# Kernel tuning notes

Hardware: AMD Instinct MI355X
Metric: run time of the kernel (lower is better)

Reference implementation:

```python
import jax, jax.numpy as jnp
import numpy as np

MAXLEN, BATCH, LATENT = 128, 32, 64
DT = 0.1
NSTEPS = 10  # steps = tf.range(0, 1, delta=DT)
HID = 32


def setup_inputs() -> dict:
    key = jax.random.key(0)
    k1, k2, k3 = jax.random.split(key, 3)
    embeddings = jax.random.normal(k1, (BATCH, MAXLEN, LATENT), dtype=jnp.float32)
    # score model: flatten(xt) ++ time -> Dense(32, relu) -> Dense(latent)
    W1 = jax.random.normal(k2, (MAXLEN * LATENT + 1, HID), dtype=jnp.float32) * 0.01
    b1 = jnp.zeros((HID,), jnp.float32)
    W2 = jax.random.normal(k3, (HID, LATENT), dtype=jnp.float32) * 0.001
    b2 = jnp.zeros((LATENT,), jnp.float32)
    return {"embeddings": embeddings, "W1": W1, "b1": b1, "W2": W2, "b2": b2}


def _score_fn(xt, t, W1, b1, W2, b2):
    # xt: (B', L, D), t: (B', 1) -> score (B', D)
    h = jnp.concatenate([xt.reshape(xt.shape[0], -1), t], axis=-1)
    h = jax.nn.relu(h @ W1 + b1)
    return h @ W2 + b2


def _forward(embeddings, W1, b1, W2, b2):
    L, B, D = MAXLEN, BATCH, LATENT
    idx = jnp.arange(L)
    emb_tr = jnp.transpose(embeddings, (1, 0, 2))                    # (L, B, D)
    # vectorized_masking (include=True): mask[t, j] = j < t
    mask = (idx[None, :] < idx[:, None]).astype(embeddings.dtype)    # (L_t, L_j)
    masked = mask[:, :, None, None] * emb_tr[None]                   # (L, L, B, D)
    score_input = masked.reshape(L, L * B, D).transpose(1, 0, 2)     # (L*B, L, D)
    labels = masked[idx, idx]                                        # (L, B, D) diagonal (zeros by construction)
    flat_pos = jnp.arange(B)[None, :] * L + idx[:, None]             # (L, B): index b*L + i

    def step(carry, xs):
        xt, error = carry
        t_val, key = xs
        t = jnp.full((L * B, 1), 1.0, embeddings.dtype) * t_val
        score = _score_fn(xt, t, W1, b1, W2, b2)                     # (L*B, D)
        snorm = jnp.linalg.norm(score)
        dW = jax.random.normal(key, (L * B, D), dtype=embeddings.dtype) * jnp.sqrt(jnp.asarray(DT, embeddings.dtype))
        dx = 0.5 * score * DT + snorm * dW
        xt_tr = xt.transpose(1, 0, 2)                                # (L, L*B, D)
        # update_slice_by_gather for every step i: xt_tr[i, b*L+i] += dx[b*L+i]
        xt_upd = xt_tr.at[idx[:, None], flat_pos].add(dx[flat_pos])  # (L, L*B, D)
        preds = xt_upd.reshape(L, L, B, D)[idx, idx]                 # gather_diagonal_slices -> (L, B, D)
        error = error + jnp.mean((labels - preds) ** 2, axis=-1)     # (L, B)
        return (xt_upd.transpose(1, 0, 2), error), None

    times = jnp.arange(NSTEPS, dtype=embeddings.dtype) * DT
    keys = jax.random.split(jax.random.key(42), NSTEPS)
    init = (score_input, jnp.zeros((L, B), embeddings.dtype))
    (xt_fin, error), _ = jax.lax.scan(step, init, (times, keys))
    xt = xt_fin.reshape(L, L, B, D)[idx, idx].transpose(1, 0, 2)     # (B, L, D)
    step_loss = jnp.sum(error)
    sequence_loss = jnp.mean(jnp.abs(embeddings - xt))
    return xt, step_loss, sequence_loss


def reference(embeddings, W1, b1, W2, b2):
    return _forward(embeddings, W1, b1, W2, b2)
```

## Files before the change

### kernel.cpp

```cpp
#include <hip/hip_runtime.h>
#include <stdint.h>

#define THREEFRY_PARTITIONABLE 1

#define DEV_HOST __host__ __device__

namespace {
constexpr int kNS      = 10;
constexpr int kSamples = 4096;
constexpr int kElems   = 262144;

constexpr int OFF_SUF   = 0;
constexpr int OFF_BASE  = 262144;
constexpr int OFF_U     = 393216;
constexpr int OFF_SCORE = 655360;
constexpr int OFF_SNRM  = 917504;
constexpr int OFF_LOSS  = 917514;
constexpr int WS_FLOATS = 917516;
}

DEV_HOST inline void tf2x32(uint32_t k0, uint32_t k1, uint32_t x0, uint32_t x1,
                            uint32_t& o0, uint32_t& o1) {
  const uint32_t k2 = k0 ^ k1 ^ 0x1BD11BDAu;
#define TF_R(r) { x0 += x1; x1 = (x1 << (r)) | (x1 >> (32 - (r))); x1 ^= x0; }
  x0 += k0; x1 += k1;
  TF_R(13) TF_R(15) TF_R(26) TF_R(6)
  x0 += k1; x1 += k2 + 1u;
  TF_R(17) TF_R(29) TF_R(16) TF_R(24)
  x0 += k2; x1 += k0 + 2u;
  TF_R(13) TF_R(15) TF_R(26) TF_R(6)
  x0 += k0; x1 += k1 + 3u;
  TF_R(17) TF_R(29) TF_R(16) TF_R(24)
  x0 += k1; x1 += k2 + 4u;
  TF_R(13) TF_R(15) TF_R(26) TF_R(6)
  x0 += k2; x1 += k0 + 5u;
#undef TF_R
  o0 = x0; o1 = x1;
}

__device__ inline uint32_t rand_bits(uint32_t key0, uint32_t key1, uint32_t idx) {
#if THREEFRY_PARTITIONABLE
  uint32_t y0, y1;
  tf2x32(key0, key1, 0u, idx, y0, y1);
  return y0 ^ y1;
#else
  const uint32_t half = kElems / 2;
  uint32_t y0, y1;
  if (idx < half) { tf2x32(key0, key1, idx, half + idx, y0, y1); return y0; }
  tf2x32(key0, key1, idx - half, idx, y0, y1);
  return y1;
#endif
}

__device__ inline float erfinv_xla(float x) {
  float w = -log1pf(-x * x);
  float p;
  if (w < 5.0f) {
    w = w - 2.5f;
    p = 2.81022636e-08f;
    p = fmaf(p, w, 3.43273939e-07f);
    p = fmaf(p, w, -3.5233877e-06f);
    p = fmaf(p, w, -4.39150654e-06f);
    p = fmaf(p, w, 0.00021858087f);
    p = fmaf(p, w, -0.00125372503f);
    p = fmaf(p, w, -0.00417768164f);
    p = fmaf(p, w, 0.246640727f);
    p = fmaf(p, w, 1.50140941f);
  } else {
    w = sqrtf(w) - 3.0f;
    p = -0.000200214257f;
    p = fmaf(p, w, 0.000100950558f);
    p = fmaf(p, w, 0.00134934322f);
    p = fmaf(p, w, -0.00367342844f);
    p = fmaf(p, w, 0.00573950773f);
    p = fmaf(p, w, -0.0076224613f);
    p = fmaf(p, w, 0.00943887047f);
    p = fmaf(p, w, 1.00167406f);
    p = fmaf(p, w, 2.83297682f);
  }
  return p * x;
}

__device__ inline float bits_to_normal(uint32_t bits) {
  const float lo = -0.99999994039535522f;
  float f = __uint_as_float((bits >> 9) | 0x3f800000u) - 1.0f;
  float u = fmaxf(lo, f * 2.0f + lo);
  return 1.41421356237309515f * erfinv_xla(u);
}

__global__ __launch_bounds__(256) void k_suffix(const float* __restrict__ W1,
                                                float* __restrict__ S) {
  const int p = blockIdx.x * 256 + threadIdx.x;
  if (p >= 2048) return;
  const int d = p >> 5, h = p & 31;
  float acc = 0.0f;
  S[(127 * 64 + d) * 32 + h] = 0.0f;
  for (int j = 126; j >= 0; --j) {
    acc += W1[((j + 1) * 64 + d) * 32 + h];
    S[(j * 64 + d) * 32 + h] = acc;
  }
}

__global__ __launch_bounds__(256) void k_base(const float* __restrict__ emb,
                                              const float* __restrict__ S,
                                              const float* __restrict__ b1,
                                              float* __restrict__ base) {
  const int tid = blockIdx.x * 256 + threadIdx.x;
  const int s = tid >> 5, h = tid & 31;
  const int j = s >> 5, b = s & 31;
  const float* e = emb + (b * 128 + j) * 64;
  float acc = b1[h];
  for (int d = 0; d < 64; ++d)
    acc = fmaf(e[d], S[(j * 64 + d) * 32 + h], acc);
  base[s * 32 + h] = acc;
}

__global__ __launch_bounds__(256) void k_step(
    const float* __restrict__ base, float* __restrict__ u,
    const float* __restrict__ W1, const float* __restrict__ W2,
    const float* __restrict__ b2, float* __restrict__ score,
    float* __restrict__ snorm_acc, float* __restrict__ loss_acc,
    int k, float tval, uint32_t key0, uint32_t key1) {
  __shared__ float u_sh[8][64];
  __shared__ float h_sh[8][32];
  __shared__ float wsum[4];
  const int tid = threadIdx.x;
  const int s0 = blockIdx.x * 8;

  if (k > 0) {
    const float snorm = sqrtf(snorm_acc[k - 1]);
#pragma unroll
    for (int r = 0; r < 2; ++r) {
      const int off = r * 256 + tid;
      const int e = s0 * 64 + off;
      const int s = s0 + (off >> 6);
      const float n = bits_to_normal(rand_bits(key0, key1, (uint32_t)e));
      const float dW = n * 0.31622776601683794f;
      const float dx = score[e] * 0.05f + snorm * dW;
      const float un = u[e] + dx;
      u[e] = un;
      u_sh[off >> 6][off & 63] = un;
      if ((s & 127) == (s >> 5)) {
        float sq = un * un;
#pragma unroll
        for (int o = 32; o > 0; o >>= 1) sq += __shfl_down(sq, o);
        if ((tid & 63) == 0) atomicAdd(&loss_acc[0], sq * (1.0f / 64.0f));
      }
    }
  } else {
#pragma unroll
    for (int r = 0; r < 2; ++r) {
      const int off = r * 256 + tid;
      u_sh[off >> 6][off & 63] = u[s0 * 64 + off];
    }
  }
  __syncthreads();

  {
    const int sl = tid >> 5, h = tid & 31;
    const int s = s0 + sl;
    const float* w1r = W1 + ((s & 127) * 64) * 32 + h;
    float pre = base[s * 32 + h] + tval * W1[8192 * 32 + h];
#pragma unroll 16
    for (int d = 0; d < 64; ++d)
      pre = fmaf(u_sh[sl][d], w1r[d * 32], pre);
    h_sh[sl][h] = fmaxf(pre, 0.0f);
  }
  __syncthreads();

  {
    const int sl = tid >> 5, c = tid & 31;
    const int s = s0 + sl;
    float sc0 = b2[c], sc1 = b2[c + 32];
#pragma unroll
    for (int hh = 0; hh < 32; ++hh) {
      const float hv = h_sh[sl][hh];
      sc0 = fmaf(hv, W2[hh * 64 + c], sc0);
      sc1 = fmaf(hv, W2[hh * 64 + c + 32], sc1);
    }
    score[s * 64 + c] = sc0;
    score[s * 64 + c + 32] = sc1;
    float sq = fmaf(sc0, sc0, sc1 * sc1);
#pragma unroll
    for (int o = 32; o > 0; o >>= 1) sq += __shfl_down(sq, o);
    if ((tid & 63) == 0) wsum[tid >> 6] = sq;
  }
  __syncthreads();
  if (tid == 0) atomicAdd(snorm_acc + k, wsum[0] + wsum[1] + wsum[2] + wsum[3]);
}

__global__ __launch_bounds__(256) void k_last(
    float* __restrict__ u, const float* __restrict__ score,
    const float* __restrict__ snorm_acc, float* __restrict__ loss_acc,
    uint32_t key0, uint32_t key1) {
  const int e = blockIdx.x * 256 + threadIdx.x;
  const int s = e >> 6;
  const float snorm = sqrtf(snorm_acc[kNS - 1]);
  const float n = bits_to_normal(rand_bits(key0, key1, (uint32_t)e));
  const float dx = score[e] * 0.05f + snorm * (n * 0.31622776601683794f);
  const float un = u[e] + dx;
  u[e] = un;
  if ((s & 127) == (s >> 5)) {
    float sq = un * un;
#pragma unroll
    for (int o = 32; o > 0; o >>= 1) sq += __shfl_down(sq, o);
    if ((threadIdx.x & 63) == 0) atomicAdd(&loss_acc[0], sq * (1.0f / 64.0f));
  }
}

__global__ __launch_bounds__(256) void k_final(const float* __restrict__ emb,
                                               const float* __restrict__ u,
                                               float* __restrict__ out,
                                               float* __restrict__ loss_acc) {
  const int g = blockIdx.x * 256 + threadIdx.x;
  const int d = g & 63, bi = g >> 6, i = bi & 127, b = bi >> 7;
  const int m = i * 32 + b;
  const int bp = m >> 7, t = m & 127;
  const int s = i * 32 + bp;
  float v = 0.0f;
  if (i < t) v = emb[(bp * 128 + i) * 64 + d];
  if ((s & 127) == t) v += u[s * 64 + d];
  out[g] = v;
  float ad = fabsf(emb[g] - v);
#pragma unroll
  for (int o = 32; o > 0; o >>= 1) ad += __shfl_down(ad, o);
  __shared__ float wsum[4];
  if ((threadIdx.x & 63) == 0) wsum[threadIdx.x >> 6] = ad;
  __syncthreads();
  if (threadIdx.x == 0) atomicAdd(&loss_acc[1], wsum[0] + wsum[1] + wsum[2] + wsum[3]);
}

__global__ void k_write(float* __restrict__ out, const float* __restrict__ loss_acc) {
  if (threadIdx.x == 0 && blockIdx.x == 0) {
    out[262144] = loss_acc[0];
    out[262145] = loss_acc[1] * (1.0f / 262144.0f);
  }
}

static void compute_step_keys(uint32_t keys[kNS][2]) {
#if THREEFRY_PARTITIONABLE
  for (int i = 0; i < kNS; ++i) {
    uint32_t y0, y1;
    tf2x32(0u, 42u, 0u, (uint32_t)i, y0, y1);
    keys[i][0] = y0; keys[i][1] = y1;
  }
#else
  uint32_t a[kNS], b[kNS], outw[2 * kNS];
  for (int i = 0; i < kNS; ++i)
    tf2x32(0u, 42u, (uint32_t)i, (uint32_t)(kNS + i), a[i], b[i]);
  for (int i = 0; i < kNS; ++i) { outw[i] = a[i]; outw[kNS + i] = b[i]; }
  for (int i = 0; i < kNS; ++i) { keys[i][0] = outw[2 * i]; keys[i][1] = outw[2 * i + 1]; }
#endif
}

extern "C" void kernel_launch(void* const* d_in, const int* in_sizes, int n_in,
                              void* d_out, int out_size, void* d_ws, size_t ws_size,
                              hipStream_t stream) {
  (void)in_sizes; (void)n_in; (void)out_size; (void)ws_size;
  const float* emb = (const float*)d_in[0];
  const float* W1  = (const float*)d_in[1];
  const float* b1  = (const float*)d_in[2];
  const float* W2  = (const float*)d_in[3];
  const float* b2  = (const float*)d_in[4];
  float* out = (float*)d_out;
  float* ws  = (float*)d_ws;

  float* S     = ws + OFF_SUF;
  float* base  = ws + OFF_BASE;
  float* u     = ws + OFF_U;
  float* score = ws + OFF_SCORE;
  float* snrm  = ws + OFF_SNRM;
  float* loss  = ws + OFF_LOSS;

  uint32_t keys[kNS][2];
  compute_step_keys(keys);

  hipMemsetAsync(u, 0, (size_t)(WS_FLOATS - OFF_U) * sizeof(float), stream);

  k_suffix<<<8, 256, 0, stream>>>(W1, S);
  k_base<<<512, 256, 0, stream>>>(emb, S, b1, base);

  for (int k = 0; k < kNS; ++k) {
    const float tval = (float)k * 0.1f;
    const uint32_t pk0 = (k > 0) ? keys[k - 1][0] : 0u;
    const uint32_t pk1 = (k > 0) ? keys[k - 1][1] : 0u;
    k_step<<<512, 256, 0, stream>>>(base, u, W1, W2, b2, score, snrm, loss,
                                    k, tval, pk0, pk1);
  }
  k_last<<<1024, 256, 0, stream>>>(u, score, snrm, loss, keys[kNS - 1][0], keys[kNS - 1][1]);
  k_final<<<1024, 256, 0, stream>>>(emb, u, out, loss);
  k_write<<<1, 64, 0, stream>>>(out, loss);
}
```

Baseline: 216.9 us.

## Fuse all SDE steps into one persistent kernel with software grid barriers

Replaces the per-step launches, the base/last/final/write kernels and the memset with one persistent 512-block kernel. Each block keeps its W1 slice, base projection and state u in registers across the ten steps. Software grid barriers built on atomic counters synchronise the global score norm between steps. The final gather and loss reduction also run inside the kernel, which removes launch overhead and the global round-trips of score and u. It relies on all 512 blocks being co-resident (launch_bounds 256,2 on a many-CU GPU); if they are not, the barrier deadlocks, and the 64-float register array per thread raises register pressure.

```diff
diff --git a/kernel.cpp b/kernel.cpp
--- a/kernel.cpp
+++ b/kernel.cpp
@@ -6,17 +6,17 @@
 #define DEV_HOST __host__ __device__
 
 namespace {
-constexpr int kNS      = 10;
-constexpr int kSamples = 4096;
-constexpr int kElems   = 262144;
-
-constexpr int OFF_SUF   = 0;
-constexpr int OFF_BASE  = 262144;
-constexpr int OFF_U     = 393216;
-constexpr int OFF_SCORE = 655360;
-constexpr int OFF_SNRM  = 917504;
-constexpr int OFF_LOSS  = 917514;
-constexpr int WS_FLOATS = 917516;
+constexpr int kNS = 10;
+constexpr int kNB = 512;
+
+constexpr int OFF_SUF     = 0;
+constexpr int OFF_U       = 262144;
+constexpr int OFF_SNRM    = 524288;
+constexpr int OFF_BAR     = 524300;
+constexpr int BAR_UINTS   = 12 * 8 * 16;
+constexpr int OFF_LOSSBLK = OFF_BAR + BAR_UINTS;
+constexpr int ZACC_N      = 12 + BAR_UINTS;
+constexpr int WS_FLOATS   = OFF_LOSSBLK + 2 * kNB;
 }
 
 DEV_HOST inline void tf2x32(uint32_t k0, uint32_t k1, uint32_t x0, uint32_t x1,
@@ -44,7 +44,7 @@
   tf2x32(key0, key1, 0u, idx, y0, y1);
   return y0 ^ y1;
 #else
-  const uint32_t half = kElems / 2;
+  const uint32_t half = 262144u / 2;
   uint32_t y0, y1;
   if (idx < half) { tf2x32(key0, key1, idx, half + idx, y0, y1); return y0; }
   tf2x32(key0, key1, idx - half, idx, y0, y1);
@@ -88,9 +88,33 @@
   return 1.41421356237309515f * erfinv_xla(u);
 }
 
+__device__ inline void gridbar(unsigned* b8, unsigned nblk, bool wait) {
+  __syncthreads();
+  if (threadIdx.x == 0) {
+    __threadfence();
+    __hip_atomic_fetch_add(b8 + (blockIdx.x & 7) * 16, 1u,
+                           __ATOMIC_RELEASE, __HIP_MEMORY_SCOPE_AGENT);
+    if (wait) {
+      for (;;) {
+        unsigned tot = 0;
+#pragma unroll
+        for (int i = 0; i < 8; ++i)
+          tot += __hip_atomic_load(b8 + i * 16, __ATOMIC_RELAXED,
+                                   __HIP_MEMORY_SCOPE_AGENT);
+        if (tot >= nblk) break;
+        __builtin_amdgcn_s_sleep(1);
+      }
+      __threadfence();
+    }
+  }
+  __syncthreads();
+}
+
 __global__ __launch_bounds__(256) void k_suffix(const float* __restrict__ W1,
-                                                float* __restrict__ S) {
+                                                float* __restrict__ S,
+                                                float* __restrict__ zacc) {
   const int p = blockIdx.x * 256 + threadIdx.x;
+  if (p < ZACC_N) zacc[p] = 0.0f;
   if (p >= 2048) return;
   const int d = p >> 5, h = p & 31;
   float acc = 0.0f;
@@ -101,139 +125,142 @@
   }
 }
 
-__global__ __launch_bounds__(256) void k_base(const float* __restrict__ emb,
-                                              const float* __restrict__ S,
-                                              const float* __restrict__ b1,
-                                              float* __restrict__ base) {
-  const int tid = blockIdx.x * 256 + threadIdx.x;
-  const int s = tid >> 5, h = tid & 31;
-  const int j = s >> 5, b = s & 31;
-  const float* e = emb + (b * 128 + j) * 64;
-  float acc = b1[h];
-  for (int d = 0; d < 64; ++d)
-    acc = fmaf(e[d], S[(j * 64 + d) * 32 + h], acc);
-  base[s * 32 + h] = acc;
-}
-
-__global__ __launch_bounds__(256) void k_step(
-    const float* __restrict__ base, float* __restrict__ u,
-    const float* __restrict__ W1, const float* __restrict__ W2,
-    const float* __restrict__ b2, float* __restrict__ score,
-    float* __restrict__ snorm_acc, float* __restrict__ loss_acc,
-    int k, float tval, uint32_t key0, uint32_t key1) {
+struct FusedParams {
+  const float* S;
+  const float* emb;
+  const float* W1;
+  const float* b1;
+  const float* W2;
+  const float* b2;
+  float* u;
+  float* out;
+  float* snrm;
+  float* lossblk;
+  unsigned* bar;
+  uint32_t key0[kNS];
+  uint32_t key1[kNS];
+};
+
+__global__ __launch_bounds__(256, 2) void k_fused(FusedParams p) {
   __shared__ float u_sh[8][64];
   __shared__ float h_sh[8][32];
   __shared__ float wsum[4];
+  __shared__ float wsumB[4];
   const int tid = threadIdx.x;
-  const int s0 = blockIdx.x * 8;
-
-  if (k > 0) {
-    const float snorm = sqrtf(snorm_acc[k - 1]);
-#pragma unroll
-    for (int r = 0; r < 2; ++r) {
-      const int off = r * 256 + tid;
-      const int e = s0 * 64 + off;
-      const int s = s0 + (off >> 6);
-      const float n = bits_to_normal(rand_bits(key0, key1, (uint32_t)e));
-      const float dW = n * 0.31622776601683794f;
-      const float dx = score[e] * 0.05f + snorm * dW;
-      const float un = u[e] + dx;
-      u[e] = un;
-      u_sh[off >> 6][off & 63] = un;
-      if ((s & 127) == (s >> 5)) {
-        float sq = un * un;
-#pragma unroll
-        for (int o = 32; o > 0; o >>= 1) sq += __shfl_down(sq, o);
-        if ((tid & 63) == 0) atomicAdd(&loss_acc[0], sq * (1.0f / 64.0f));
-      }
-    }
-  } else {
-#pragma unroll
-    for (int r = 0; r < 2; ++r) {
-      const int off = r * 256 + tid;
-      u_sh[off >> 6][off & 63] = u[s0 * 64 + off];
-    }
-  }
-  __syncthreads();
-
+  const int blk = blockIdx.x;
+  const unsigned nb = gridDim.x;
+  const int s0 = blk * 8;
+  const int sl = tid >> 5, c = tid & 31;
+  const int s = s0 + sl;
+  const int jw = s & 127;
+  const bool contrib = (jw == (s >> 5));
+
+  float w1reg[64];
   {
-    const int sl = tid >> 5, h = tid & 31;
-    const int s = s0 + sl;
-    const float* w1r = W1 + ((s & 127) * 64) * 32 + h;
-    float pre = base[s * 32 + h] + tval * W1[8192 * 32 + h];
+    const float* w1r = p.W1 + (jw * 64) * 32 + c;
+#pragma unroll
+    for (int d = 0; d < 64; ++d) w1reg[d] = w1r[d * 32];
+  }
+  const float w1t  = p.W1[8192 * 32 + c];
+  const float b2_0 = p.b2[c], b2_1 = p.b2[c + 32];
+
+  float basev;
+  {
+    const int jj = s >> 5, bb = s & 31;
+    const float* e  = p.emb + (bb * 128 + jj) * 64;
+    const float* Sp = p.S + (jj * 64) * 32 + c;
+    float acc = p.b1[c];
 #pragma unroll 16
-    for (int d = 0; d < 64; ++d)
-      pre = fmaf(u_sh[sl][d], w1r[d * 32], pre);
-    h_sh[sl][h] = fmaxf(pre, 0.0f);
-  }
-  __syncthreads();
-
-  {
-    const int sl = tid >> 5, c = tid & 31;
-    const int s = s0 + sl;
-    float sc0 = b2[c], sc1 = b2[c + 32];
+    for (int d = 0; d < 64; ++d) acc = fmaf(e[d], Sp[d * 32], acc);
+    basev = acc;
+  }
+
+  float u0 = 0.0f, u1 = 0.0f;
+  float lacc = 0.0f;
+
+  for (int k = 0; k < kNS; ++k) {
+    u_sh[sl][c]      = u0;
+    u_sh[sl][c + 32] = u1;
+    __syncthreads();
+    const float tval = (float)k * 0.1f;
+    float pre = fmaf(tval, w1t, basev);
+#pragma unroll
+    for (int d = 0; d < 64; ++d) pre = fmaf(u_sh[sl][d], w1reg[d], pre);
+    h_sh[sl][c] = fmaxf(pre, 0.0f);
+    __syncthreads();
+    float sc0 = b2_0, sc1 = b2_1;
 #pragma unroll
     for (int hh = 0; hh < 32; ++hh) {
       const float hv = h_sh[sl][hh];
-      sc0 = fmaf(hv, W2[hh * 64 + c], sc0);
-      sc1 = fmaf(hv, W2[hh * 64 + c + 32], sc1);
-    }
-    score[s * 64 + c] = sc0;
-    score[s * 64 + c + 32] = sc1;
+      sc0 = fmaf(hv, p.W2[hh * 64 + c], sc0);
+      sc1 = fmaf(hv, p.W2[hh * 64 + c + 32], sc1);
+    }
     float sq = fmaf(sc0, sc0, sc1 * sc1);
 #pragma unroll
     for (int o = 32; o > 0; o >>= 1) sq += __shfl_down(sq, o);
     if ((tid & 63) == 0) wsum[tid >> 6] = sq;
-  }
+    const uint32_t e0 = (uint32_t)(s * 64 + c);
+    const float n0 = bits_to_normal(rand_bits(p.key0[k], p.key1[k], e0));
+    const float n1 = bits_to_normal(rand_bits(p.key0[k], p.key1[k], e0 + 32u));
+    __syncthreads();
+    if (tid == 0) atomicAdd(p.snrm + k, wsum[0] + wsum[1] + wsum[2] + wsum[3]);
+    gridbar(p.bar + k * 128, nb, true);
+    const float snorm = sqrtf(__hip_atomic_load(p.snrm + k, __ATOMIC_RELAXED,
+                                                __HIP_MEMORY_SCOPE_AGENT));
+    u0 = u0 + (sc0 * 0.05f + snorm * (n0 * 0.31622776601683794f));
+    u1 = u1 + (sc1 * 0.05f + snorm * (n1 * 0.31622776601683794f));
+    if (contrib) lacc = fmaf(u0, u0, fmaf(u1, u1, lacc));
+  }
+
+  p.u[s * 64 + c]      = u0;
+  p.u[s * 64 + c + 32] = u1;
+  gridbar(p.bar + kNS * 128, nb, true);
+
+  float lsum = 0.0f;
+#pragma unroll
+  for (int r = 0; r < 2; ++r) {
+    const int g = blk * 256 + tid + r * 131072;
+    const int d = g & 63, bi = g >> 6, i = bi & 127, b = bi >> 7;
+    const int m = i * 32 + b;
+    const int bp = m >> 7, t = m & 127;
+    const int ss = i * 32 + bp;
+    float v = 0.0f;
+    if (i < t) v = p.emb[(bp * 128 + i) * 64 + d];
+    if ((ss & 127) == t) v += p.u[ss * 64 + d];
+    p.out[g] = v;
+    lsum += fabsf(p.emb[g] - v);
+  }
+  float la = lacc * (1.0f / 64.0f);
+#pragma unroll
+  for (int o = 32; o > 0; o >>= 1) {
+    la   += __shfl_down(la, o);
+    lsum += __shfl_down(lsum, o);
+  }
+  if ((tid & 63) == 0) { wsum[tid >> 6] = la; wsumB[tid >> 6] = lsum; }
   __syncthreads();
-  if (tid == 0) atomicAdd(snorm_acc + k, wsum[0] + wsum[1] + wsum[2] + wsum[3]);
-}
-
-__global__ __launch_bounds__(256) void k_last(
-    float* __restrict__ u, const float* __restrict__ score,
-    const float* __restrict__ snorm_acc, float* __restrict__ loss_acc,
-    uint32_t key0, uint32_t key1) {
-  const int e = blockIdx.x * 256 + threadIdx.x;
-  const int s = e >> 6;
-  const float snorm = sqrtf(snorm_acc[kNS - 1]);
-  const float n = bits_to_normal(rand_bits(key0, key1, (uint32_t)e));
-  const float dx = score[e] * 0.05f + snorm * (n * 0.31622776601683794f);
-  const float un = u[e] + dx;
-  u[e] = un;
-  if ((s & 127) == (s >> 5)) {
-    float sq = un * un;
-#pragma unroll
-    for (int o = 32; o > 0; o >>= 1) sq += __shfl_down(sq, o);
-    if ((threadIdx.x & 63) == 0) atomicAdd(&loss_acc[0], sq * (1.0f / 64.0f));
-  }
-}
-
-__global__ __launch_bounds__(256) void k_final(const float* __restrict__ emb,
-                                               const float* __restrict__ u,
-                                               float* __restrict__ out,
-                                               float* __restrict__ loss_acc) {
-  const int g = blockIdx.x * 256 + threadIdx.x;
-  const int d = g & 63, bi = g >> 6, i = bi & 127, b = bi >> 7;
-  const int m = i * 32 + b;
-  const int bp = m >> 7, t = m & 127;
-  const int s = i * 32 + bp;
-  float v = 0.0f;
-  if (i < t) v = emb[(bp * 128 + i) * 64 + d];
-  if ((s & 127) == t) v += u[s * 64 + d];
-  out[g] = v;
-  float ad = fabsf(emb[g] - v);
-#pragma unroll
-  for (int o = 32; o > 0; o >>= 1) ad += __shfl_down(ad, o);
-  __shared__ float wsum[4];
-  if ((threadIdx.x & 63) == 0) wsum[threadIdx.x >> 6] = ad;
-  __syncthreads();
-  if (threadIdx.x == 0) atomicAdd(&loss_acc[1], wsum[0] + wsum[1] + wsum[2] + wsum[3]);
-}
-
-__global__ void k_write(float* __restrict__ out, const float* __restrict__ loss_acc) {
-  if (threadIdx.x == 0 && blockIdx.x == 0) {
-    out[262144] = loss_acc[0];
-    out[262145] = loss_acc[1] * (1.0f / 262144.0f);
+  if (tid == 0) {
+    p.lossblk[2 * blk]     = wsum[0] + wsum[1] + wsum[2] + wsum[3];
+    p.lossblk[2 * blk + 1] = wsumB[0] + wsumB[1] + wsumB[2] + wsumB[3];
+  }
+
+  gridbar(p.bar + (kNS + 1) * 128, nb, blk == 0);
+  if (blk == 0) {
+    float a = 0.0f, m = 0.0f;
+    for (int q = tid; q < kNB; q += 256) {
+      a += p.lossblk[2 * q];
+      m += p.lossblk[2 * q + 1];
+    }
+#pragma unroll
+    for (int o = 32; o > 0; o >>= 1) {
+      a += __shfl_down(a, o);
+      m += __shfl_down(m, o);
+    }
+    if ((tid & 63) == 0) { wsum[tid >> 6] = a; wsumB[tid >> 6] = m; }
+    __syncthreads();
+    if (tid == 0) {
+      p.out[262144] = wsum[0] + wsum[1] + wsum[2] + wsum[3];
+      p.out[262145] = (wsumB[0] + wsumB[1] + wsumB[2] + wsumB[3]) * (1.0f / 262144.0f);
+    }
   }
 }
 
@@ -265,29 +292,21 @@
   float* out = (float*)d_out;
   float* ws  = (float*)d_ws;
 
-  float* S     = ws + OFF_SUF;
-  float* base  = ws + OFF_BASE;
-  float* u     = ws + OFF_U;
-  float* score = ws + OFF_SCORE;
-  float* snrm  = ws + OFF_SNRM;
-  float* loss  = ws + OFF_LOSS;
+  float* S       = ws + OFF_SUF;
+  float* u       = ws + OFF_U;
+  float* snrm    = ws + OFF_SNRM;
+  float* lossblk = ws + OFF_LOSSBLK;
+  unsigned* bar  = (unsigned*)(ws + OFF_BAR);
 
   uint32_t keys[kNS][2];
   compute_step_keys(keys);
 
-  hipMemsetAsync(u, 0, (size_t)(WS_FLOATS - OFF_U) * sizeof(float), stream);
-
-  k_suffix<<<8, 256, 0, stream>>>(W1, S);
-  k_base<<<512, 256, 0, stream>>>(emb, S, b1, base);
-
-  for (int k = 0; k < kNS; ++k) {
-    const float tval = (float)k * 0.1f;
-    const uint32_t pk0 = (k > 0) ? keys[k - 1][0] : 0u;
-    const uint32_t pk1 = (k > 0) ? keys[k - 1][1] : 0u;
-    k_step<<<512, 256, 0, stream>>>(base, u, W1, W2, b2, score, snrm, loss,
-                                    k, tval, pk0, pk1);
-  }
-  k_last<<<1024, 256, 0, stream>>>(u, score, snrm, loss, keys[kNS - 1][0], keys[kNS - 1][1]);
-  k_final<<<1024, 256, 0, stream>>>(emb, u, out, loss);
-  k_write<<<1, 64, 0, stream>>>(out, loss);
-}
+  k_suffix<<<8, 256, 0, stream>>>(W1, S, snrm);
+
+  FusedParams p;
+  p.S = S; p.emb = emb; p.W1 = W1; p.b1 = b1; p.W2 = W2; p.b2 = b2;
+  p.u = u; p.out = out; p.snrm = snrm; p.lossblk = lossblk; p.bar = bar;
+  for (int i = 0; i < kNS; ++i) { p.key0[i] = keys[i][0]; p.key1[i] = keys[i][1]; }
+
+  k_fused<<<kNB, 256, 0, stream>>>(p);
+}
```

New measurement: 562.5 us. 159% more time.
